# Performance work log

Hardware: AMD Instinct MI355X
Metric: run time of the kernel (lower is better)

The kernel has to match this reference:

```python
import jax, jax.numpy as jnp
import numpy as np

E = 64      # routed experts
K = 2       # top-k
CAP = 1024


def setup_inputs() -> dict:
    key = jax.random.key(0)
    ks = jax.random.split(key, 5)
    S, B, D, DFF = 2048, 4, 1024, 1408
    x = jax.random.normal(ks[0], (S, B, D), jnp.float32)
    Wg = jax.random.normal(ks[1], (D, E), jnp.float32) * 0.02
    W1 = jax.random.normal(ks[2], (E, D, DFF), jnp.float32) * 0.02
    W3 = jax.random.normal(ks[3], (E, D, DFF), jnp.float32) * 0.02
    W2 = jax.random.normal(ks[4], (E, DFF, D), jnp.float32) * 0.02
    return {"x": x, "Wg": Wg, "W1": W1, "W3": W3, "W2": W2}


def _moe(x, Wg, W1, W3, W2):
    S, B, D = x.shape
    tokens = jnp.transpose(x, (1, 0, 2)).reshape(-1, D)       # [T, D], T = B*S
    T = tokens.shape[0]

    # --- gate: softmax -> top-k, renormalize, aux loss (GShard-style) ---
    logits = tokens @ Wg                                       # [T, E]
    probs = jax.nn.softmax(logits, axis=-1)
    topk_w, topk_idx = jax.lax.top_k(probs, K)                 # [T, K]
    topk_w = topk_w / jnp.sum(topk_w, axis=-1, keepdims=True)
    me = jnp.mean(probs, axis=0)                               # [E] mean prob
    ce = jnp.mean(jax.nn.one_hot(topk_idx, E, dtype=jnp.float32).sum(1), axis=0) / K
    l_aux = E * jnp.sum(me * ce)

    # --- dispatch: per-pair slot within its expert via cumsum of one-hots ---
    flat_e = topk_idx.reshape(-1)                              # [T*K]
    oh = jax.nn.one_hot(flat_e, E, dtype=jnp.int32)            # [T*K, E]
    pos = jnp.cumsum(oh, axis=0) - 1                           # slot per expert
    slot = jnp.take_along_axis(pos, flat_e[:, None], axis=1)[:, 0]  # [T*K]
    keep = slot < CAP
    slot = jnp.where(keep, slot, 0)
    xr = jnp.repeat(tokens, K, axis=0)                         # [T*K, D]
    xr = jnp.where(keep[:, None], xr, 0.0)
    buf = jnp.zeros((E, CAP, D), x.dtype).at[flat_e, slot].add(xr)  # [E, C, D]

    # --- grouped expert FFN: SiLU-gated MLP per expert ---
    h = jax.nn.silu(jnp.einsum('ecd,edf->ecf', buf, W1)) * jnp.einsum('ecd,edf->ecf', buf, W3)
    eo = jnp.einsum('ecf,efd->ecd', h, W2)                     # [E, C, D]

    # --- combine: gather back, weight by gate probs, sum over k ---
    gathered = eo[flat_e, slot] * keep[:, None].astype(x.dtype)  # [T*K, D]
    combined = jnp.sum(gathered.reshape(T, K, D) * topk_w[..., None], axis=1)
    y = jnp.transpose(combined.reshape(B, S, D), (1, 0, 2))    # back to [S, B, D]
    return y, l_aux


def reference(x, Wg, W1, W3, W2):
    return _moe(x, Wg, W1, W3, W2)
```

## Files before the change

### kernel.cpp

```cpp
#include <hip/hip_runtime.h>
#include <hip/hip_bf16.h>


#define S_ 2048
#define B_ 4
#define D_ 1024
#define DFF_ 1408
#define E_ 64
#define T_ 8192
#define KTOP_ 2
#define NPAIR_ (T_*KTOP_)
#define PAD_ 384
#define ROWS_ (E_*PAD_)

#define BM 128
#define BN 64
#define BK 32

typedef __attribute__((ext_vector_type(8))) short short8;
typedef __attribute__((ext_vector_type(4))) short s16x4;
typedef __attribute__((ext_vector_type(4))) float f32x4;
typedef __attribute__((ext_vector_type(4))) unsigned short us4;

constexpr size_t OFF_PROBS  = 0;
constexpr size_t OFF_PE     = OFF_PROBS + (size_t)T_*E_*4;
constexpr size_t OFF_PW     = OFF_PE + (size_t)NPAIR_*4;
constexpr size_t OFF_COUNTS = OFF_PW + (size_t)NPAIR_*4;
constexpr size_t OFF_CURSOR = OFF_COUNTS + 256;
constexpr size_t OFF_MESUM  = OFF_CURSOR + 256;
constexpr size_t OFF_ROWTOK = OFF_MESUM + 256;
constexpr size_t OFF_ROWW   = OFF_ROWTOK + (size_t)ROWS_*4;
constexpr size_t OFF_XBUF   = OFF_ROWW + (size_t)ROWS_*4;
constexpr size_t OFF_H      = OFF_XBUF + (size_t)ROWS_*D_*2;

__device__ __forceinline__ short f2bfs(float f) {
  union { __hip_bfloat16 h; short s; } u;
  u.h = __float2bfloat16(f);
  return u.s;
}

__device__ __forceinline__ int SWZ(int g) { return g ^ (((g >> 4) & 3) << 1); }

#define BAR() do {                                   \
    __builtin_amdgcn_sched_barrier(0);               \
    __builtin_amdgcn_s_barrier();                    \
    __builtin_amdgcn_sched_barrier(0);               \
  } while (0)
#define WAIT_LGKM0() asm volatile("s_waitcnt lgkmcnt(0)" ::: "memory")

__device__ __forceinline__ float softmax64(float acc, int lane) {
  float m = acc;
  for (int o = 32; o; o >>= 1) m = fmaxf(m, __shfl_xor(m, o));
  float p = expf(acc - m);
  float s = p;
  for (int o = 32; o; o >>= 1) s += __shfl_xor(s, o);
  return p / s;
}

__device__ __forceinline__ void topk_write(float p, int t, int lane,
    float* __restrict__ probs, int* __restrict__ pe, float* __restrict__ pw,
    int* __restrict__ counts) {
  probs[(size_t)t * E_ + lane] = p;
  float v1 = p; int i1 = lane;
  for (int o = 32; o; o >>= 1) {
    float ov = __shfl_xor(v1, o); int oi = __shfl_xor(i1, o);
    if (ov > v1 || (ov == v1 && oi < i1)) { v1 = ov; i1 = oi; }
  }
  float v2 = (lane == i1) ? -1.f : p; int i2 = lane;
  for (int o = 32; o; o >>= 1) {
    float ov = __shfl_xor(v2, o); int oi = __shfl_xor(i2, o);
    if (ov > v2 || (ov == v2 && oi < i2)) { v2 = ov; i2 = oi; }
  }
  if (lane == 0) {
    float wsum = v1 + v2;
    pe[2 * t]     = i1; pw[2 * t]     = v1 / wsum;
    pe[2 * t + 1] = i2; pw[2 * t + 1] = v2 / wsum;
    atomicAdd(&counts[i1], 1);
    atomicAdd(&counts[i2], 1);
  }
}

__global__ __launch_bounds__(256) void gate_kernel(
    const float* __restrict__ x, const float* __restrict__ Wg,
    float* __restrict__ probs, int* __restrict__ pe, float* __restrict__ pw,
    int* __restrict__ counts) {
  int t0 = blockIdx.x * 8;
  int tid = threadIdx.x;
  int lane = tid & 63, wv = tid >> 6;
  __shared__ float tk[8][D_];
  for (int u = tid; u < 8 * (D_ / 4); u += 256) {
    int r = u >> 8, c4 = u & 255;
    int t = t0 + r;
    int b = t >> 11, s = t & (S_ - 1);
    ((float4*)tk[r])[c4] = ((const float4*)(x + (size_t)(s * B_ + b) * D_))[c4];
  }
  __syncthreads();
  const float* tkA = tk[2 * wv];
  const float* tkB = tk[2 * wv + 1];
  float acc0 = 0.f, acc1 = 0.f;
  #pragma unroll 8
  for (int d = 0; d < D_; ++d) {
    float w = Wg[(size_t)d * E_ + lane];
    acc0 += tkA[d] * w;
    acc1 += tkB[d] * w;
  }
  int ta = t0 + 2 * wv, tb = ta + 1;
  float p0 = softmax64(acc0, lane);
  float p1 = softmax64(acc1, lane);
  topk_write(p0, ta, lane, probs, pe, pw, counts);
  topk_write(p1, tb, lane, probs, pe, pw, counts);
}

__global__ __launch_bounds__(256) void me_kernel(const float* __restrict__ probs,
                                                 float* __restrict__ mesum) {
  int e = blockIdx.x, tid = threadIdx.x;
  float a = 0.f;
  for (int t = tid; t < T_; t += 256) a += probs[(size_t)t * E_ + e];
  __shared__ float red[256];
  red[tid] = a; __syncthreads();
  for (int s = 128; s; s >>= 1) {
    if (tid < s) red[tid] += red[tid + s];
    __syncthreads();
  }
  if (tid == 0) mesum[e] = red[0];
}

__global__ __launch_bounds__(64) void finalize_kernel(
    const int* __restrict__ counts, const float* __restrict__ mesum,
    float* __restrict__ laux_out) {
  int lane = threadIdx.x;
  float contrib = (mesum[lane] / (float)T_) * ((float)counts[lane] / (float)(T_ * KTOP_));
  for (int o = 32; o; o >>= 1) contrib += __shfl_xor(contrib, o);
  if (lane == 0) laux_out[0] = (float)E_ * contrib;
}

__global__ __launch_bounds__(64) void scatter_kernel(
    const float* __restrict__ x, const int* __restrict__ pe, const float* __restrict__ pw,
    int* __restrict__ cursor, int* __restrict__ rowtok, float* __restrict__ roww,
    unsigned short* __restrict__ xbufO) {
  int p = blockIdx.x;
  int lane = threadIdx.x;
  __shared__ int srow;
  __shared__ int sexp;
  if (lane == 0) {
    int e = pe[p];
    int slot = atomicAdd(&cursor[e], 1);
    int row = (slot < PAD_) ? slot : -1;
    if (row >= 0) { rowtok[e * PAD_ + row] = p >> 1; roww[e * PAD_ + row] = pw[p]; }
    srow = row; sexp = e;
  }
  __syncthreads();
  int m = srow;
  if (m < 0) return;
  int e = sexp;
  int t = p >> 1;
  int b = t >> 11, s = t & (S_ - 1);
  const float4* src = (const float4*)(x + (size_t)(s * B_ + b) * D_);
  unsigned short* dstE = xbufO + (size_t)e * D_ * PAD_;
  #pragma unroll
  for (int oo = 0; oo < 2; ++oo) {
    int o = lane + oo * 64;
    float4 lo = src[o * 2], hi = src[o * 2 + 1];
    short8 g;
    g[0] = f2bfs(lo.x); g[1] = f2bfs(lo.y); g[2] = f2bfs(lo.z); g[3] = f2bfs(lo.w);
    g[4] = f2bfs(hi.x); g[5] = f2bfs(hi.y); g[6] = f2bfs(hi.z); g[7] = f2bfs(hi.w);
    *(short8*)(dstE + ((size_t)o * PAD_ + m) * 8) = g;
  }
}

__global__ __launch_bounds__(256, 3) void ffn1_kernel(
    const unsigned short* __restrict__ xbufO, const float* __restrict__ W1,
    const float* __restrict__ W3, const int* __restrict__ counts,
    unsigned short* __restrict__ hO) {
  int bid = blockIdx.x;
  int r = bid & 7, u = bid >> 3;
  int mb = u % 3; int v = u / 3;
  int ni = v % 22; int eg = v / 22;
  int e = eg * 8 + r;
  int n0 = ni * BN;
  int m0 = mb * BM;
  int Me = min(counts[e], PAD_);
  if (m0 >= Me) return;

  const unsigned short* AO = xbufO + (size_t)e * D_ * PAD_;
  const float* B1p = W1 + (size_t)e * D_ * DFF_ + n0;
  const float* B3p = W3 + (size_t)e * D_ * DFF_ + n0;
  unsigned short* hE = hO + (size_t)e * PAD_ * DFF_;

  __shared__ short B1s[2 * BK * BN];
  __shared__ short B3s[2 * BK * BN];
  __shared__ short Hb[BM * BN];

  int tid = threadIdx.x;
  int lane = tid & 63;
  int wv = tid >> 6, wr = wv >> 1, wc = wv & 1;

  int msel = tid >> 7;
  int t7 = tid & 127;
  int bcol = t7 & 63, khalf = t7 >> 6;
  const float* qB = (msel ? B3p : B1p) + (size_t)(khalf * 8) * DFF_ + bcol;
  char* Bdst = (char*)(msel ? B3s : B1s);
  int boff0 = ((bcol >> 4) << 10) + (SWZ((khalf << 4) + (bcol & 15)) << 4);
  int boff1 = ((bcol >> 4) << 10) + (SWZ(((khalf + 2) << 4) + (bcol & 15)) << 4);

  const unsigned short* qa =
      AO + (((size_t)(lane >> 4)) * PAD_ + m0 + (wr << 6) + (lane & 15)) * 8;

  short8 afE[4], afO[4];
  float fBE[16], fBO[16];
  f32x4 acc1[4][2] = {};
  f32x4 acc3[4][2] = {};

#define F1_ALOAD(SET) do {                                               \
    _Pragma("unroll")                                                    \
    for (int mi = 0; mi < 4; ++mi)                                       \
      af##SET[mi] = *(const short8*)(qa + mi * 128);                     \
    qa += (size_t)4 * PAD_ * 8;                                          \
  } while (0)

#define F1_BLOAD(SET) do {                                               \
    _Pragma("unroll")                                                    \
    for (int j = 0; j < 8; ++j) {                                        \
      fB##SET[j]     = qB[(size_t)j * DFF_];                             \
      fB##SET[8 + j] = qB[(size_t)(16 + j) * DFF_];                      \
    }                                                                    \
    qB += (size_t)BK * DFF_;                                             \
  } while (0)

#define F1_BWRITE(SET, BUF) do {                                         \
    short8 s0, s1;                                                       \
    _Pragma("unroll")                                                    \
    for (int j = 0; j < 8; ++j) {                                        \
      s0[j] = f2bfs(fB##SET[j]); s1[j] = f2bfs(fB##SET[8 + j]);          \
    }                                                                    \
    *(short8*)(Bdst + (BUF)*4096 + boff0) = s0;                          \
    *(short8*)(Bdst + (BUF)*4096 + boff1) = s1;                          \
  } while (0)

#define F1_MFMA(BUF, SET) do {                                           \
    int lsw = SWZ(lane) << 4;                                            \
    __builtin_amdgcn_s_setprio(1);                                       \
    _Pragma("unroll")                                                    \
    for (int q = 0; q < 2; ++q) {                                        \
      short8 bf1 = *(const short8*)((char*)B1s + (BUF)*4096 + (((wc << 1) + q) << 10) + lsw); \
      short8 bf3 = *(const short8*)((char*)B3s + (BUF)*4096 + (((wc << 1) + q) << 10) + lsw); \
      _Pragma("unroll")                                                  \
      for (int mi = 0; mi < 4; ++mi) {                                   \
        acc1[mi][q] = __builtin_amdgcn_mfma_f32_16x16x32_bf16(af##SET[mi], bf1, acc1[mi][q], 0, 0, 0); \
        acc3[mi][q] = __builtin_amdgcn_mfma_f32_16x16x32_bf16(af##SET[mi], bf3, acc3[mi][q], 0, 0, 0); \
      }                                                                  \
    }                                                                    \
    __builtin_amdgcn_s_setprio(0);                                       \
  } while (0)

  F1_ALOAD(E); F1_BLOAD(E);
  F1_ALOAD(O); F1_BLOAD(O);
  for (int it = 0; it < 15; ++it) {
    F1_BWRITE(E, 0); WAIT_LGKM0(); BAR();
    F1_MFMA(0, E);
    BAR();
    F1_ALOAD(E); F1_BLOAD(E);
    F1_BWRITE(O, 1); WAIT_LGKM0(); BAR();
    F1_MFMA(1, O);
    BAR();
    F1_ALOAD(O); F1_BLOAD(O);
  }
  F1_BWRITE(E, 0); WAIT_LGKM0(); BAR(); F1_MFMA(0, E); BAR();
  F1_BWRITE(O, 1); WAIT_LGKM0(); BAR(); F1_MFMA(1, O);

  __syncthreads();
  int lr = (lane >> 4) << 2, lc = lane & 15;
  #pragma unroll
  for (int mi = 0; mi < 4; ++mi) {
    #pragma unroll
    for (int j = 0; j < 4; ++j) {
      int m = ((wr << 2) + mi) * 16 + lr + j;
      #pragma unroll
      for (int q = 0; q < 2; ++q) {
        int c = (wc << 5) + (q << 4) + lc;
        float a = acc1[mi][q][j];
        float gt = a / (1.f + __expf(-a));
        Hb[((c >> 3) * BM + m) * 8 + (c & 7)] = f2bfs(gt * acc3[mi][q][j]);
      }
    }
  }
  __syncthreads();
  int co = tid >> 5, ml0 = (tid & 31) << 2;
  size_t fo = (size_t)(n0 >> 3) + co;
  #pragma unroll
  for (int i = 0; i < 4; ++i) {
    int ml = ml0 + i;
    short8 vq = *(const short8*)(Hb + ((size_t)co * BM + ml) * 8);
    *(short8*)(hE + (fo * PAD_ + m0 + ml) * 8) = vq;
  }
}

__global__ __launch_bounds__(256, 4) void ffn2_kernel(
    const unsigned short* __restrict__ hO, const float* __restrict__ W2,
    const int* __restrict__ counts, const int* __restrict__ rowtok,
    const float* __restrict__ roww, float* __restrict__ y) {
  int bid = blockIdx.x;
  int r = bid & 7, u = bid >> 3;
  int mb = u % 3; int v = u / 3;
  int ni = v % 16; int eg = v / 16;
  int e = eg * 8 + r;
  int n0 = ni * BN;
  int m0 = mb * BM;
  int Me = min(counts[e], PAD_);
  if (m0 >= Me) return;

  const unsigned short* AO = hO + (size_t)e * PAD_ * DFF_;
  const float* Bw = W2 + (size_t)e * DFF_ * D_ + n0;

  __shared__ short Bs[2 * BK * BN];

  int tid = threadIdx.x;
  int lane = tid & 63;
  int wv = tid >> 6, wr = wv >> 1, wc = wv & 1;

  int bcol = lane, kseg = wv;
  const float* qB = Bw + (size_t)(kseg * 8) * D_ + bcol;
  int boff = ((bcol >> 4) << 10) + (SWZ((kseg << 4) + (bcol & 15)) << 4);

  const unsigned short* qa =
      AO + (((size_t)(lane >> 4)) * PAD_ + m0 + (wr << 6) + (lane & 15)) * 8;

  short8 afE[4], afO[4];
  float fBE[8], fBO[8];
  f32x4 acc[4][2] = {};

#define F2_ALOAD(SET) do {                                               \
    _Pragma("unroll")                                                    \
    for (int mi = 0; mi < 4; ++mi)                                       \
      af##SET[mi] = *(const short8*)(qa + mi * 128);                     \
    qa += (size_t)4 * PAD_ * 8;                                          \
  } while (0)

#define F2_BLOAD(SET) do {                                               \
    _Pragma("unroll")                                                    \
    for (int j = 0; j < 8; ++j) fB##SET[j] = qB[(size_t)j * D_];         \
    qB += (size_t)BK * D_;                                               \
  } while (0)

#define F2_BWRITE(SET, BUF) do {                                         \
    short8 sb;                                                           \
    _Pragma("unroll")                                                    \
    for (int j = 0; j < 8; ++j) sb[j] = f2bfs(fB##SET[j]);               \
    *(short8*)((char*)Bs + (BUF)*4096 + boff) = sb;                      \
  } while (0)

#define F2_MFMA(BUF, SET) do {                                           \
    int lsw = SWZ(lane) << 4;                                            \
    __builtin_amdgcn_s_setprio(1);                                       \
    _Pragma("unroll")                                                    \
    for (int q = 0; q < 2; ++q) {                                        \
      short8 bfr = *(const short8*)((char*)Bs + (BUF)*4096 + (((wc << 1) + q) << 10) + lsw); \
      _Pragma("unroll")                                                  \
      for (int mi = 0; mi < 4; ++mi)                                     \
        acc[mi][q] = __builtin_amdgcn_mfma_f32_16x16x32_bf16(af##SET[mi], bfr, acc[mi][q], 0, 0, 0); \
    }                                                                    \
    __builtin_amdgcn_s_setprio(0);                                       \
  } while (0)

  F2_ALOAD(E); F2_BLOAD(E);
  F2_ALOAD(O); F2_BLOAD(O);
  for (int it = 0; it < 21; ++it) {
    F2_BWRITE(E, 0); WAIT_LGKM0(); BAR();
    F2_MFMA(0, E);
    BAR();
    F2_ALOAD(E); F2_BLOAD(E);
    F2_BWRITE(O, 1); WAIT_LGKM0(); BAR();
    F2_MFMA(1, O);
    BAR();
    F2_ALOAD(O); F2_BLOAD(O);
  }
  F2_BWRITE(E, 0); WAIT_LGKM0(); BAR(); F2_MFMA(0, E); BAR();
  F2_BWRITE(O, 1); WAIT_LGKM0(); BAR(); F2_MFMA(1, O);

  int lr = (lane >> 4) << 2, lc = lane & 15;
  #pragma unroll
  for (int mi = 0; mi < 4; ++mi) {
    #pragma unroll
    for (int j = 0; j < 4; ++j) {
      int m = m0 + ((wr << 2) + mi) * 16 + lr + j;
      if (m < Me) {
        int rw = e * PAD_ + m;
        int t = rowtok[rw];
        float w = roww[rw];
        int b = t >> 11, s = t & (S_ - 1);
        float* yp = y + (size_t)(s * B_ + b) * D_ + n0 + (wc << 5) + lc;
        #pragma unroll
        for (int q = 0; q < 2; ++q)
          atomicAdd(&yp[q << 4], w * acc[mi][q][j]);
      }
    }
  }
}

extern "C" void kernel_launch(void* const* d_in, const int* in_sizes, int n_in,
                              void* d_out, int out_size, void* d_ws, size_t ws_size,
                              hipStream_t stream) {
  const float* x  = (const float*)d_in[0];
  const float* Wg = (const float*)d_in[1];
  const float* W1 = (const float*)d_in[2];
  const float* W3 = (const float*)d_in[3];
  const float* W2 = (const float*)d_in[4];
  float* y = (float*)d_out;
  float* laux = y + (size_t)S_ * B_ * D_;

  char* ws = (char*)d_ws;
  float* probs  = (float*)(ws + OFF_PROBS);
  int*   pe     = (int*)  (ws + OFF_PE);
  float* pw     = (float*)(ws + OFF_PW);
  int*   counts = (int*)  (ws + OFF_COUNTS);
  int*   cursor = (int*)  (ws + OFF_CURSOR);
  float* mesum  = (float*)(ws + OFF_MESUM);
  int*   rowtok = (int*)  (ws + OFF_ROWTOK);
  float* roww   = (float*)(ws + OFF_ROWW);
  unsigned short* xbufO = (unsigned short*)(ws + OFF_XBUF);
  unsigned short* hO    = (unsigned short*)(ws + OFF_H);

  hipMemsetAsync(d_out, 0, (size_t)out_size * sizeof(float), stream);
  hipMemsetAsync(counts, 0, 512, stream);

  gate_kernel<<<T_ / 8, 256, 0, stream>>>(x, Wg, probs, pe, pw, counts);
  me_kernel<<<E_, 256, 0, stream>>>(probs, mesum);
  finalize_kernel<<<1, 64, 0, stream>>>(counts, mesum, laux);
  scatter_kernel<<<NPAIR_, 64, 0, stream>>>(x, pe, pw, cursor, rowtok, roww, xbufO);
  ffn1_kernel<<<8 * 8 * 22 * 3, 256, 0, stream>>>(xbufO, W1, W3, counts, hO);
  ffn2_kernel<<<8 * 8 * 16 * 3, 256, 0, stream>>>(hO, W2, counts, rowtok, roww, y);
}
```

Measured before the change: 701.5 us.

## Triple-buffer B tiles in FFN kernels, drop trailing barrier per k-step

Both FFN GEMM kernels move from two to three LDS buffers for the converted weight tiles, with three register sets of prefetched B values. The second barrier after each MFMA step is removed, since with three buffers a buffer is not rewritten until two steps later. The aim is fewer barriers per k-iteration and a deeper global-load prefetch. In exchange it uses more LDS and registers, which may lower occupancy under launch_bounds(256,4), and a third B register set is held live.

```diff
diff --git a/kernel.cpp b/kernel.cpp
--- a/kernel.cpp
+++ b/kernel.cpp
@@ -18,7 +18,6 @@
 #define BK 32
 
 typedef __attribute__((ext_vector_type(8))) short short8;
-typedef __attribute__((ext_vector_type(4))) short s16x4;
 typedef __attribute__((ext_vector_type(4))) float f32x4;
 typedef __attribute__((ext_vector_type(4))) unsigned short us4;
 
@@ -187,8 +186,8 @@
   const float* B3p = W3 + (size_t)e * D_ * DFF_ + n0;
   unsigned short* hE = hO + (size_t)e * PAD_ * DFF_;
 
-  __shared__ short B1s[2 * BK * BN];
-  __shared__ short B3s[2 * BK * BN];
+  __shared__ short B1s[3 * BK * BN];
+  __shared__ short B3s[3 * BK * BN];
   __shared__ short Hb[BM * BN];
 
   int tid = threadIdx.x;
@@ -207,37 +206,37 @@
       AO + (((size_t)(lane >> 4)) * PAD_ + m0 + (wr << 6) + (lane & 15)) * 8;
 
   short8 afE[4], afO[4];
-  float fBE[16], fBO[16];
+  float fBP[16], fBQ[16], fBR[16];
   f32x4 acc1[4][2] = {};
   f32x4 acc3[4][2] = {};
 
-#define F1_ALOAD(SET) do {                                               \
+#define F1_ALOAD(AS) do {                                                \
     _Pragma("unroll")                                                    \
     for (int mi = 0; mi < 4; ++mi)                                       \
-      af##SET[mi] = *(const short8*)(qa + mi * 128);                     \
+      af##AS[mi] = *(const short8*)(qa + mi * 128);                      \
     qa += (size_t)4 * PAD_ * 8;                                          \
   } while (0)
 
-#define F1_BLOAD(SET) do {                                               \
+#define F1_BLOAD(BS) do {                                                \
     _Pragma("unroll")                                                    \
     for (int j = 0; j < 8; ++j) {                                        \
-      fB##SET[j]     = qB[(size_t)j * DFF_];                             \
-      fB##SET[8 + j] = qB[(size_t)(16 + j) * DFF_];                      \
+      fB##BS[j]     = qB[(size_t)j * DFF_];                              \
+      fB##BS[8 + j] = qB[(size_t)(16 + j) * DFF_];                       \
     }                                                                    \
     qB += (size_t)BK * DFF_;                                             \
   } while (0)
 
-#define F1_BWRITE(SET, BUF) do {                                         \
+#define F1_BWRITE(BS, BUF) do {                                          \
     short8 s0, s1;                                                       \
     _Pragma("unroll")                                                    \
     for (int j = 0; j < 8; ++j) {                                        \
-      s0[j] = f2bfs(fB##SET[j]); s1[j] = f2bfs(fB##SET[8 + j]);          \
+      s0[j] = f2bfs(fB##BS[j]); s1[j] = f2bfs(fB##BS[8 + j]);            \
     }                                                                    \
     *(short8*)(Bdst + (BUF)*4096 + boff0) = s0;                          \
     *(short8*)(Bdst + (BUF)*4096 + boff1) = s1;                          \
   } while (0)
 
-#define F1_MFMA(BUF, SET) do {                                           \
+#define F1_MFMA(BUF, AS) do {                                            \
     int lsw = SWZ(lane) << 4;                                            \
     __builtin_amdgcn_s_setprio(1);                                       \
     _Pragma("unroll")                                                    \
@@ -246,27 +245,36 @@
       short8 bf3 = *(const short8*)((char*)B3s + (BUF)*4096 + (((wc << 1) + q) << 10) + lsw); \
       _Pragma("unroll")                                                  \
       for (int mi = 0; mi < 4; ++mi) {                                   \
-        acc1[mi][q] = __builtin_amdgcn_mfma_f32_16x16x32_bf16(af##SET[mi], bf1, acc1[mi][q], 0, 0, 0); \
-        acc3[mi][q] = __builtin_amdgcn_mfma_f32_16x16x32_bf16(af##SET[mi], bf3, acc3[mi][q], 0, 0, 0); \
+        acc1[mi][q] = __builtin_amdgcn_mfma_f32_16x16x32_bf16(af##AS[mi], bf1, acc1[mi][q], 0, 0, 0); \
+        acc3[mi][q] = __builtin_amdgcn_mfma_f32_16x16x32_bf16(af##AS[mi], bf3, acc3[mi][q], 0, 0, 0); \
       }                                                                  \
     }                                                                    \
     __builtin_amdgcn_s_setprio(0);                                       \
   } while (0)
 
-  F1_ALOAD(E); F1_BLOAD(E);
-  F1_ALOAD(O); F1_BLOAD(O);
-  for (int it = 0; it < 15; ++it) {
-    F1_BWRITE(E, 0); WAIT_LGKM0(); BAR();
-    F1_MFMA(0, E);
-    BAR();
-    F1_ALOAD(E); F1_BLOAD(E);
-    F1_BWRITE(O, 1); WAIT_LGKM0(); BAR();
-    F1_MFMA(1, O);
-    BAR();
-    F1_ALOAD(O); F1_BLOAD(O);
-  }
-  F1_BWRITE(E, 0); WAIT_LGKM0(); BAR(); F1_MFMA(0, E); BAR();
-  F1_BWRITE(O, 1); WAIT_LGKM0(); BAR(); F1_MFMA(1, O);
+#define F1_STEP(BS, BUF, AS) do {                                        \
+    F1_BWRITE(BS, BUF); WAIT_LGKM0(); BAR();                             \
+    F1_MFMA(BUF, AS);                                                    \
+  } while (0)
+
+  F1_ALOAD(E); F1_ALOAD(O);
+  F1_BLOAD(P); F1_BLOAD(Q); F1_BLOAD(R);
+  for (int it = 0; it < 4; ++it) {
+    F1_STEP(P, 0, E); F1_ALOAD(E); F1_BLOAD(P);
+    F1_STEP(Q, 1, O); F1_ALOAD(O); F1_BLOAD(Q);
+    F1_STEP(R, 2, E); F1_ALOAD(E); F1_BLOAD(R);
+    F1_STEP(P, 0, O); F1_ALOAD(O); F1_BLOAD(P);
+    F1_STEP(Q, 1, E); F1_ALOAD(E); F1_BLOAD(Q);
+    F1_STEP(R, 2, O); F1_ALOAD(O); F1_BLOAD(R);
+  }
+  F1_STEP(P, 0, E); F1_ALOAD(E); F1_BLOAD(P);
+  F1_STEP(Q, 1, O); F1_ALOAD(O); F1_BLOAD(Q);
+  F1_STEP(R, 2, E); F1_ALOAD(E); F1_BLOAD(R);
+  F1_STEP(P, 0, O); F1_ALOAD(O); F1_BLOAD(P);
+  F1_STEP(Q, 1, E); F1_ALOAD(E); F1_BLOAD(Q);
+  F1_STEP(R, 2, O); F1_ALOAD(O);
+  F1_STEP(P, 0, E);
+  F1_STEP(Q, 1, O);
 
   __syncthreads();
   int lr = (lane >> 4) << 2, lc = lane & 15;
@@ -312,7 +320,7 @@
   const unsigned short* AO = hO + (size_t)e * PAD_ * DFF_;
   const float* Bw = W2 + (size_t)e * DFF_ * D_ + n0;
 
-  __shared__ short Bs[2 * BK * BN];
+  __shared__ short Bs[3 * BK * BN];
 
   int tid = threadIdx.x;
   int lane = tid & 63;
@@ -326,30 +334,30 @@
       AO + (((size_t)(lane >> 4)) * PAD_ + m0 + (wr << 6) + (lane & 15)) * 8;
 
   short8 afE[4], afO[4];
-  float fBE[8], fBO[8];
+  float fBP[8], fBQ[8], fBR[8];
   f32x4 acc[4][2] = {};
 
-#define F2_ALOAD(SET) do {                                               \
+#define F2_ALOAD(AS) do {                                                \
     _Pragma("unroll")                                                    \
     for (int mi = 0; mi < 4; ++mi)                                       \
-      af##SET[mi] = *(const short8*)(qa + mi * 128);                     \
+      af##AS[mi] = *(const short8*)(qa + mi * 128);                      \
     qa += (size_t)4 * PAD_ * 8;                                          \
   } while (0)
 
-#define F2_BLOAD(SET) do {                                               \
-    _Pragma("unroll")                                                    \
-    for (int j = 0; j < 8; ++j) fB##SET[j] = qB[(size_t)j * D_];         \
+#define F2_BLOAD(BS) do {                                                \
+    _Pragma("unroll")                                                    \
+    for (int j = 0; j < 8; ++j) fB##BS[j] = qB[(size_t)j * D_];          \
     qB += (size_t)BK * D_;                                               \
   } while (0)
 
-#define F2_BWRITE(SET, BUF) do {                                         \
+#define F2_BWRITE(BS, BUF) do {                                          \
     short8 sb;                                                           \
     _Pragma("unroll")                                                    \
-    for (int j = 0; j < 8; ++j) sb[j] = f2bfs(fB##SET[j]);               \
+    for (int j = 0; j < 8; ++j) sb[j] = f2bfs(fB##BS[j]);                \
     *(short8*)((char*)Bs + (BUF)*4096 + boff) = sb;                      \
   } while (0)
 
-#define F2_MFMA(BUF, SET) do {                                           \
+#define F2_MFMA(BUF, AS) do {                                            \
     int lsw = SWZ(lane) << 4;                                            \
     __builtin_amdgcn_s_setprio(1);                                       \
     _Pragma("unroll")                                                    \
@@ -357,25 +365,34 @@
       short8 bfr = *(const short8*)((char*)Bs + (BUF)*4096 + (((wc << 1) + q) << 10) + lsw); \
       _Pragma("unroll")                                                  \
       for (int mi = 0; mi < 4; ++mi)                                     \
-        acc[mi][q] = __builtin_amdgcn_mfma_f32_16x16x32_bf16(af##SET[mi], bfr, acc[mi][q], 0, 0, 0); \
+        acc[mi][q] = __builtin_amdgcn_mfma_f32_16x16x32_bf16(af##AS[mi], bfr, acc[mi][q], 0, 0, 0); \
     }                                                                    \
     __builtin_amdgcn_s_setprio(0);                                       \
   } while (0)
 
-  F2_ALOAD(E); F2_BLOAD(E);
-  F2_ALOAD(O); F2_BLOAD(O);
-  for (int it = 0; it < 21; ++it) {
-    F2_BWRITE(E, 0); WAIT_LGKM0(); BAR();
-    F2_MFMA(0, E);
-    BAR();
-    F2_ALOAD(E); F2_BLOAD(E);
-    F2_BWRITE(O, 1); WAIT_LGKM0(); BAR();
-    F2_MFMA(1, O);
-    BAR();
-    F2_ALOAD(O); F2_BLOAD(O);
-  }
-  F2_BWRITE(E, 0); WAIT_LGKM0(); BAR(); F2_MFMA(0, E); BAR();
-  F2_BWRITE(O, 1); WAIT_LGKM0(); BAR(); F2_MFMA(1, O);
+#define F2_STEP(BS, BUF, AS) do {                                        \
+    F2_BWRITE(BS, BUF); WAIT_LGKM0(); BAR();                             \
+    F2_MFMA(BUF, AS);                                                    \
+  } while (0)
+
+  F2_ALOAD(E); F2_ALOAD(O);
+  F2_BLOAD(P); F2_BLOAD(Q); F2_BLOAD(R);
+  for (int it = 0; it < 6; ++it) {
+    F2_STEP(P, 0, E); F2_ALOAD(E); F2_BLOAD(P);
+    F2_STEP(Q, 1, O); F2_ALOAD(O); F2_BLOAD(Q);
+    F2_STEP(R, 2, E); F2_ALOAD(E); F2_BLOAD(R);
+    F2_STEP(P, 0, O); F2_ALOAD(O); F2_BLOAD(P);
+    F2_STEP(Q, 1, E); F2_ALOAD(E); F2_BLOAD(Q);
+    F2_STEP(R, 2, O); F2_ALOAD(O); F2_BLOAD(R);
+  }
+  F2_STEP(P, 0, E); F2_ALOAD(E); F2_BLOAD(P);
+  F2_STEP(Q, 1, O); F2_ALOAD(O); F2_BLOAD(Q);
+  F2_STEP(R, 2, E); F2_ALOAD(E); F2_BLOAD(R);
+  F2_STEP(P, 0, O); F2_ALOAD(O); F2_BLOAD(P);
+  F2_STEP(Q, 1, E); F2_ALOAD(E); F2_BLOAD(Q);
+  F2_STEP(R, 2, O); F2_ALOAD(O);
+  F2_STEP(P, 0, E);
+  F2_STEP(Q, 1, O);
 
   int lr = (lane >> 4) << 2, lc = lane & 15;
   #pragma unroll
```

Result: slower. 991.6 us (+41.4%).
